# Performance work log

Hardware: AMD Instinct MI355X
Metric: run time of the kernel (lower is better)

The kernel has to match this reference:

```python
import jax, jax.numpy as jnp
import numpy as np

N_NODES = 100000


def _gcn_conv(h, src, dst, norm, W, b):
    # h: [N, F_in] -> [N, F_out]; aggregate normalized messages over edges
    h = h @ W                                   # transform first (cheaper messages)
    msg = h[src] * norm[:, None]                # [E_tot, F_out]
    agg = jax.ops.segment_sum(msg, dst, num_segments=N_NODES)
    return agg + b


def setup_inputs() -> dict:
    key = jax.random.key(0)
    k1, k2, k3, k4 = jax.random.split(key, 4)
    x = jax.random.normal(k1, (N_NODES, 256), dtype=jnp.float32)
    edge_index = jax.random.randint(k2, (2, 1600000), 0, N_NODES, dtype=jnp.int64)
    W1 = jax.random.normal(k3, (256, 128), dtype=jnp.float32) * (1.0 / np.sqrt(256))
    b1 = jnp.zeros((128,), dtype=jnp.float32)
    W2 = jax.random.normal(k4, (128, 40), dtype=jnp.float32) * (1.0 / np.sqrt(128))
    b2 = jnp.zeros((40,), dtype=jnp.float32)
    return {"x": x, "edge_index": edge_index, "W1": W1, "b1": b1, "W2": W2, "b2": b2}


def reference(x, edge_index, W1, b1, W2, b2):
    # add self-loops
    loop = jnp.arange(N_NODES, dtype=edge_index.dtype)
    src = jnp.concatenate([edge_index[0], loop])
    dst = jnp.concatenate([edge_index[1], loop])
    # symmetric normalization D^{-1/2} (A+I) D^{-1/2}
    deg = jax.ops.segment_sum(jnp.ones_like(dst, dtype=x.dtype), dst, num_segments=N_NODES)
    dinv = jax.lax.rsqrt(jnp.maximum(deg, 1.0))
    norm = dinv[src] * dinv[dst]                # [E_tot]

    h = _gcn_conv(x, src, dst, norm, W1, b1)
    h = jax.nn.relu(h)                          # dropout p=0 / eval -> identity
    h = _gcn_conv(h, src, dst, norm, W2, b2)
    return jax.nn.log_softmax(h, axis=1)
```

## Files before the change

kernel.cpp:

```cpp
#include <hip/hip_runtime.h>
#include <hip/hip_fp8.h>
#include <math.h>

#define N_NODES 100000
#define N_EDGES 1600000
#define F_IN 256
#define F_H 128
#define F_OUT 40

#define BIN_SHIFT 9
#define BIN_NODES 512
#define NBIN 196
#define CAP 12288
#define CNT_PAD 16
#define PART_CHUNK 8192
#define DEGB 64

typedef __attribute__((ext_vector_type(8))) short bf16x8;
typedef __attribute__((ext_vector_type(4))) float floatx4;
typedef __attribute__((ext_vector_type(2))) float floatx2;
typedef __attribute__((ext_vector_type(2))) unsigned int uintx2;
typedef __attribute__((ext_vector_type(4))) unsigned int uintx4;

__device__ __forceinline__ unsigned short f2bf(float f) {
    unsigned int u = __float_as_uint(f);
    u += 0x7fffu + ((u >> 16) & 1u);
    return (unsigned short)(u >> 16);
}

#if defined(__has_builtin)
#if __has_builtin(__builtin_amdgcn_cvt_pk_fp8_f32)
#define HAVE_PK_ENC 1
#endif
#if __has_builtin(__builtin_amdgcn_cvt_pk_f32_fp8)
#define HAVE_PK_DEC 1
#endif
#if __has_builtin(__builtin_amdgcn_cvt_f32_fp8)
#define HAVE_SC_DEC 1
#endif
#endif

__device__ __forceinline__ unsigned char f2f8(float f) {
#ifdef HAVE_PK_ENC
    int r = __builtin_amdgcn_cvt_pk_fp8_f32(f, f, 0, false);
    return (unsigned char)(r & 0xff);
#else
    __hip_fp8_e4m3 t(f);
    return (unsigned char)t.__x;
#endif
}
__device__ __forceinline__ float f82f(unsigned char b) {
#ifdef HAVE_SC_DEC
    return __builtin_amdgcn_cvt_f32_fp8((int)b, 0);
#else
    __hip_fp8_e4m3 t; t.__x = (__hip_fp8_storage_t)b;
    return (float)t;
#endif
}
__device__ __forceinline__ floatx2 f8x2tof(unsigned short u) {
#ifdef HAVE_PK_DEC
    return __builtin_amdgcn_cvt_pk_f32_fp8((int)u, false);
#else
    floatx2 r;
    r.x = f82f((unsigned char)(u & 0xff));
    r.y = f82f((unsigned char)(u >> 8));
    return r;
#endif
}

__device__ __forceinline__ void acc16(uintx4 u, float* a) {
#pragma unroll
    for (int d = 0; d < 4; ++d) {
        floatx2 lo = f8x2tof((unsigned short)(u[d] & 0xffffu));
        floatx2 hi = f8x2tof((unsigned short)(u[d] >> 16));
        a[d * 4 + 0] += lo.x; a[d * 4 + 1] += lo.y;
        a[d * 4 + 2] += hi.x; a[d * 4 + 3] += hi.y;
    }
}

__global__ __launch_bounds__(256) void k_part(const int* __restrict__ eidx,
                                              int* __restrict__ gcnt,
                                              unsigned int* __restrict__ parts) {
    __shared__ int hist[4][NBIN];
    __shared__ int sbase[NBIN];
    __shared__ int rcnt[NBIN];
    const int tid = threadIdx.x;
    const int wv = tid >> 6;
    for (int i = tid; i < NBIN; i += 256) {
        hist[0][i] = 0; hist[1][i] = 0; hist[2][i] = 0; hist[3][i] = 0; rcnt[i] = 0;
    }
    __syncthreads();
    const int e0 = blockIdx.x * PART_CHUNK;
    const int e1 = min(e0 + PART_CHUNK, N_EDGES);
    for (int e = e0 + tid; e < e1; e += 256) {
        int d = eidx[N_EDGES + e];
        atomicAdd(&hist[wv][d >> BIN_SHIFT], 1);
    }
    __syncthreads();
    for (int b = tid; b < NBIN; b += 256) {
        int tot = hist[0][b] + hist[1][b] + hist[2][b] + hist[3][b];
        int old = atomicAdd(&gcnt[b * CNT_PAD], tot);
        sbase[b] = b * CAP + old;
    }
    __syncthreads();
    for (int e = e0 + tid; e < e1; e += 256) {
        int d = eidx[N_EDGES + e];
        int s = eidx[e];
        int b = d >> BIN_SHIFT;
        int r = atomicAdd(&rcnt[b], 1);
        parts[sbase[b] + r] = ((unsigned int)s << BIN_SHIFT) | (unsigned int)(d & (BIN_NODES - 1));
    }
}

__global__ __launch_bounds__(256) void k_build(const unsigned int* __restrict__ parts,
                                               const int* __restrict__ gcnt,
                                               int* __restrict__ rowptr,
                                               float* __restrict__ dinv,
                                               int* __restrict__ csr_src) {
    __shared__ int deg[4][BIN_NODES];
    __shared__ int cur[BIN_NODES];
    __shared__ int scan[256];
    const int tid = threadIdx.x;
    const int wv = tid >> 6;
    const int g = blockIdx.x;

    scan[tid] = (tid < NBIN) ? gcnt[tid * CNT_PAD] : 0;
    __syncthreads();
    for (int off = 1; off < 256; off <<= 1) {
        int v = 0;
        if (tid >= off) v = scan[tid - off];
        __syncthreads();
        if (tid >= off) scan[tid] += v;
        __syncthreads();
    }
    const int binBase = (g == 0) ? 0 : scan[g - 1];
    const int cntg = scan[g] - binBase;

    for (int i = tid; i < BIN_NODES; i += 256) {
        deg[0][i] = 0; deg[1][i] = 0; deg[2][i] = 0; deg[3][i] = 0;
    }
    __syncthreads();

    const unsigned int* pp = parts + (size_t)g * CAP;
    for (int i = tid; i < cntg; i += 256)
        atomicAdd(&deg[wv][pp[i] & (BIN_NODES - 1)], 1);
    __syncthreads();

    const int n0 = 2 * tid, n1 = 2 * tid + 1;
    const int d0 = deg[0][n0] + deg[1][n0] + deg[2][n0] + deg[3][n0];
    const int d1 = deg[0][n1] + deg[1][n1] + deg[2][n1] + deg[3][n1];
    scan[tid] = d0 + d1;
    __syncthreads();
    for (int off = 1; off < 256; off <<= 1) {
        int v = 0;
        if (tid >= off) v = scan[tid - off];
        __syncthreads();
        if (tid >= off) scan[tid] += v;
        __syncthreads();
    }
    const int pre = (tid == 0) ? 0 : scan[tid - 1];
    const int p0 = binBase + pre;
    const int p1 = p0 + d0;
    const int node0 = g * BIN_NODES + n0;
    if (node0 < N_NODES)     { rowptr[node0]     = p0; dinv[node0]     = rsqrtf((float)d0 + 1.0f); }
    if (node0 + 1 < N_NODES) { rowptr[node0 + 1] = p1; dinv[node0 + 1] = rsqrtf((float)d1 + 1.0f); }
    cur[n0] = p0;
    cur[n1] = p1;
    __syncthreads();

    for (int i = tid; i < cntg; i += 256) {
        unsigned int u = pp[i];
        int pos = atomicAdd(&cur[u & (BIN_NODES - 1)], 1);
        csr_src[pos] = (int)(u >> BIN_SHIFT);
    }
    if (g == NBIN - 1 && tid == 0) rowptr[N_NODES] = N_EDGES;
}

__global__ __launch_bounds__(256) void k_dhist(const int* __restrict__ rowptr,
                                               int* __restrict__ dcnt) {
    __shared__ int h[4][DEGB];
    const int tid = threadIdx.x;
    const int wv = tid >> 6;
    if (tid < DEGB) { h[0][tid] = 0; h[1][tid] = 0; h[2][tid] = 0; h[3][tid] = 0; }
    __syncthreads();
    const int base = blockIdx.x * 1024;
#pragma unroll
    for (int j = 0; j < 4; ++j) {
        int i = base + j * 256 + tid;
        if (i < N_NODES) {
            int d = min(rowptr[i + 1] - rowptr[i], DEGB - 1);
            atomicAdd(&h[wv][d], 1);
        }
    }
    __syncthreads();
    if (tid < DEGB) {
        int tot = h[0][tid] + h[1][tid] + h[2][tid] + h[3][tid];
        if (tot) atomicAdd(&dcnt[tid * CNT_PAD], tot);
    }
}

__global__ void k_dscan(int* dcnt) {
    if (threadIdx.x == 0) {
        int run = 0;
        for (int i = 0; i < DEGB; ++i) {
            int c = dcnt[i * CNT_PAD];
            dcnt[i * CNT_PAD] = run;
            run += c;
        }
    }
}

__global__ __launch_bounds__(256) void k_dscat(const int* __restrict__ rowptr,
                                               int* __restrict__ dcnt,
                                               int* __restrict__ perm) {
    __shared__ int h[4][DEGB];
    __shared__ int base[DEGB];
    __shared__ int lr[DEGB];
    const int tid = threadIdx.x;
    const int wv = tid >> 6;
    if (tid < DEGB) {
        h[0][tid] = 0; h[1][tid] = 0; h[2][tid] = 0; h[3][tid] = 0; lr[tid] = 0;
    }
    __syncthreads();
    const int nb = blockIdx.x * 1024;
    int dg[4];
#pragma unroll
    for (int j = 0; j < 4; ++j) {
        int i = nb + j * 256 + tid;
        dg[j] = -1;
        if (i < N_NODES) {
            dg[j] = min(rowptr[i + 1] - rowptr[i], DEGB - 1);
            atomicAdd(&h[wv][dg[j]], 1);
        }
    }
    __syncthreads();
    if (tid < DEGB) {
        int tot = h[0][tid] + h[1][tid] + h[2][tid] + h[3][tid];
        base[tid] = tot ? atomicAdd(&dcnt[tid * CNT_PAD], tot) : 0;
    }
    __syncthreads();
#pragma unroll
    for (int j = 0; j < 4; ++j) {
        int i = nb + j * 256 + tid;
        if (dg[j] >= 0) {
            int r = atomicAdd(&lr[dg[j]], 1);
            perm[base[dg[j]] + r] = i;
        }
    }
}

__global__ void k_cvt_w(const float* __restrict__ W1, const float* __restrict__ W2,
                        short* __restrict__ W1t, short* __restrict__ W2t,
                        int* __restrict__ gcnt, int* __restrict__ dcnt) {
    int b = blockIdx.x, t = threadIdx.x;
    if (b < 128) {
        int idx = b * 256 + t;
        int n = idx >> 8, k = idx & 255;
        W1t[n * 256 + k] = (short)f2bf(W1[k * 128 + n]);
    } else {
        int idx = (b - 128) * 256 + t;
        if (idx < 48 * 128) {
            int n = idx >> 7, k = idx & 127;
            float v = (n < F_OUT) ? W2[k * F_OUT + n] : 0.f;
            W2t[n * 128 + k] = (short)f2bf(v);
        }
        if (idx < NBIN * CNT_PAD) gcnt[idx] = 0;
        if (idx < DEGB * CNT_PAD) dcnt[idx] = 0;
    }
}

__global__ __launch_bounds__(256) void k_gemm1_mfma(const float* __restrict__ x,
                                                    const short* __restrict__ W1t,
                                                    const float* __restrict__ dinv,
                                                    unsigned char* __restrict__ h1f8) {
    __shared__ short As[128 * 40];
    __shared__ short Bs[128 * 264];
    __shared__ float Ds[128];
    const int tid = threadIdx.x;
    const int row0 = blockIdx.x * 128;
    const int w = tid >> 6, l = tid & 63;
    const int l15 = l & 15, q = l >> 4;
    const int ar = tid >> 1;
    const int ak = (tid & 1) * 16;

    {
        const int n = tid >> 1;
        const int kh = (tid & 1) * 128;
#pragma unroll
        for (int i = 0; i < 16; ++i)
            *(bf16x8*)&Bs[n * 264 + kh + i * 8] = *(const bf16x8*)&W1t[n * 256 + kh + i * 8];
    }
    if (tid < 128) {
        int r = row0 + tid;
        Ds[tid] = (r < N_NODES) ? dinv[r] : 0.f;
    }

    floatx4 acc[2][8];
#pragma unroll
    for (int a = 0; a < 2; ++a)
#pragma unroll
        for (int nt = 0; nt < 8; ++nt) acc[a][nt] = (floatx4)0.f;

    const bool arow_ok = (row0 + ar) < N_NODES;
    const float* xp = x + (size_t)(row0 + ar) * F_IN;

    for (int k0 = 0; k0 < F_IN; k0 += 32) {
        bf16x8 av0 = (bf16x8)0, av1 = (bf16x8)0;
        if (arow_ok) {
            floatx4 f0 = *(const floatx4*)(xp + k0 + ak);
            floatx4 f1 = *(const floatx4*)(xp + k0 + ak + 4);
            floatx4 f2 = *(const floatx4*)(xp + k0 + ak + 8);
            floatx4 f3 = *(const floatx4*)(xp + k0 + ak + 12);
            av0[0] = (short)f2bf(f0[0]); av0[1] = (short)f2bf(f0[1]);
            av0[2] = (short)f2bf(f0[2]); av0[3] = (short)f2bf(f0[3]);
            av0[4] = (short)f2bf(f1[0]); av0[5] = (short)f2bf(f1[1]);
            av0[6] = (short)f2bf(f1[2]); av0[7] = (short)f2bf(f1[3]);
            av1[0] = (short)f2bf(f2[0]); av1[1] = (short)f2bf(f2[1]);
            av1[2] = (short)f2bf(f2[2]); av1[3] = (short)f2bf(f2[3]);
            av1[4] = (short)f2bf(f3[0]); av1[5] = (short)f2bf(f3[1]);
            av1[6] = (short)f2bf(f3[2]); av1[7] = (short)f2bf(f3[3]);
        }
        __syncthreads();
        *(bf16x8*)&As[ar * 40 + ak]     = av0;
        *(bf16x8*)&As[ar * 40 + ak + 8] = av1;
        __syncthreads();

        bf16x8 af[2], bfr[8];
#pragma unroll
        for (int a = 0; a < 2; ++a)
            af[a] = *(const bf16x8*)&As[((w * 2 + a) * 16 + l15) * 40 + q * 8];
#pragma unroll
        for (int nt = 0; nt < 8; ++nt)
            bfr[nt] = *(const bf16x8*)&Bs[(nt * 16 + l15) * 264 + k0 + q * 8];
#pragma unroll
        for (int a = 0; a < 2; ++a)
#pragma unroll
            for (int nt = 0; nt < 8; ++nt)
                acc[a][nt] = __builtin_amdgcn_mfma_f32_16x16x32_bf16(af[a], bfr[nt], acc[a][nt], 0, 0, 0);
    }
#pragma unroll
    for (int a = 0; a < 2; ++a) {
#pragma unroll
        for (int r = 0; r < 4; ++r) {
            const int rl = (w * 2 + a) * 16 + q * 4 + r;
            const int row = row0 + rl;
            if (row < N_NODES) {
                const float ds = Ds[rl];
                unsigned char* hp = h1f8 + (size_t)row * F_H;
#pragma unroll
                for (int nt = 0; nt < 8; ++nt)
                    hp[nt * 16 + l15] = f2f8(acc[a][nt][r] * ds);
            }
        }
    }
}

__global__ __launch_bounds__(256) void k_spmm1(const int* __restrict__ rowptr,
                                               const int* __restrict__ csr_src,
                                               const int* __restrict__ perm,
                                               const uintx4* __restrict__ h1d4,
                                               const float* __restrict__ dinv,
                                               const float* __restrict__ b1,
                                               unsigned short* __restrict__ agg1b) {
    const int slot = threadIdx.x >> 3;
    const int p = threadIdx.x & 7;
    const int gid = blockIdx.x * 32 + slot;
    const int node = perm[gid];

    const int beg = rowptr[node];
    const int end = rowptr[node + 1];
    const float dv = dinv[node];

    float accA[16], accB[16];
#pragma unroll
    for (int jj = 0; jj < 16; ++jj) { accA[jj] = 0.f; accB[jj] = 0.f; }
    acc16(h1d4[(size_t)node * 8 + p], accA);

    int i = beg;
    for (; i + 3 < end; i += 4) {
        int s0 = csr_src[i], s1 = csr_src[i + 1], s2 = csr_src[i + 2], s3 = csr_src[i + 3];
        uintx4 u0 = h1d4[(size_t)s0 * 8 + p];
        uintx4 u1 = h1d4[(size_t)s1 * 8 + p];
        uintx4 u2 = h1d4[(size_t)s2 * 8 + p];
        uintx4 u3 = h1d4[(size_t)s3 * 8 + p];
        acc16(u0, accA); acc16(u1, accB);
        acc16(u2, accA); acc16(u3, accB);
    }
    for (; i < end; ++i)
        acc16(h1d4[(size_t)csr_src[i] * 8 + p], accA);

    const float* bp = b1 + 16 * p;
    unsigned int ow[8];
#pragma unroll
    for (int jj = 0; jj < 8; ++jj) {
        float v0 = fmaf(accA[2 * jj]     + accB[2 * jj],     dv, bp[2 * jj]);
        float v1 = fmaf(accA[2 * jj + 1] + accB[2 * jj + 1], dv, bp[2 * jj + 1]);
        v0 = v0 > 0.f ? v0 : 0.f;
        v1 = v1 > 0.f ? v1 : 0.f;
        ow[jj] = ((unsigned int)f2bf(v1) << 16) | f2bf(v0);
    }
    uintx4* op = (uintx4*)(agg1b + (size_t)node * F_H) + 2 * p;
    uintx4 o0, o1;
    o0[0] = ow[0]; o0[1] = ow[1]; o0[2] = ow[2]; o0[3] = ow[3];
    o1[0] = ow[4]; o1[1] = ow[5]; o1[2] = ow[6]; o1[3] = ow[7];
    op[0] = o0;
    op[1] = o1;
}

__global__ __launch_bounds__(256) void k_gemm2_mfma(const unsigned short* __restrict__ agg1b,
                                                    const short* __restrict__ W2t,
                                                    const float* __restrict__ dinv,
                                                    unsigned char* __restrict__ h2f8) {
    __shared__ short As[128 * 40];
    __shared__ short Bs[48 * 136];
    __shared__ float Ds[128];
    const int tid = threadIdx.x;
    const int bidr = blockIdx.x;
    const int kx = bidr & 7, jx = bidr >> 3;
    const int cb = (kx < 6) ? (kx * 98 + jx) : (6 * 98 + (kx - 6) * 97 + jx);
    const int row0 = cb * 128;
    const int w = tid >> 6, l = tid & 63;
    const int l15 = l & 15, q = l >> 4;
    const int ar = tid >> 1;
    const int ak = (tid & 1) * 16;

#pragma unroll
    for (int i = 0; i < 3; ++i) {
        int c = tid * 3 + i;
        int n = c >> 4, koff = (c & 15) * 8;
        *(bf16x8*)&Bs[n * 136 + koff] = *(const bf16x8*)&W2t[n * 128 + koff];
    }
    if (tid < 128) {
        int r = row0 + tid;
        Ds[tid] = (r < N_NODES) ? dinv[r] : 0.f;
    }

    floatx4 acc[2][3];
#pragma unroll
    for (int a = 0; a < 2; ++a)
#pragma unroll
        for (int nt = 0; nt < 3; ++nt) acc[a][nt] = (floatx4)0.f;

    const bool arow_ok = (row0 + ar) < N_NODES;
    const unsigned short* ap = agg1b + (size_t)(row0 + ar) * F_H;

    for (int k0 = 0; k0 < F_H; k0 += 32) {
        bf16x8 a0, a1;
        if (arow_ok) {
            a0 = *(const bf16x8*)(ap + k0 + ak);
            a1 = *(const bf16x8*)(ap + k0 + ak + 8);
        } else {
            a0 = (bf16x8)0; a1 = (bf16x8)0;
        }
        *(bf16x8*)&As[ar * 40 + ak]     = a0;
        *(bf16x8*)&As[ar * 40 + ak + 8] = a1;
        __syncthreads();

        bf16x8 af[2], bfr[3];
#pragma unroll
        for (int a = 0; a < 2; ++a)
            af[a] = *(const bf16x8*)&As[((w * 2 + a) * 16 + l15) * 40 + q * 8];
#pragma unroll
        for (int nt = 0; nt < 3; ++nt)
            bfr[nt] = *(const bf16x8*)&Bs[(nt * 16 + l15) * 136 + k0 + q * 8];
#pragma unroll
        for (int a = 0; a < 2; ++a)
#pragma unroll
            for (int nt = 0; nt < 3; ++nt)
                acc[a][nt] = __builtin_amdgcn_mfma_f32_16x16x32_bf16(af[a], bfr[nt], acc[a][nt], 0, 0, 0);
        __syncthreads();
    }
#pragma unroll
    for (int a = 0; a < 2; ++a) {
#pragma unroll
        for (int nt = 0; nt < 3; ++nt) {
            int col = nt * 16 + l15;
#pragma unroll
            for (int r = 0; r < 4; ++r) {
                int rl = (w * 2 + a) * 16 + q * 4 + r;
                int row = row0 + rl;
                if (row < N_NODES && col < F_OUT)
                    h2f8[(size_t)row * F_OUT + col] = f2f8(acc[a][nt][r] * Ds[rl]);
            }
        }
    }
}

__global__ __launch_bounds__(256) void k_spmm2_lsm(const int* __restrict__ rowptr,
                                                   const int* __restrict__ csr_src,
                                                   const int* __restrict__ perm,
                                                   const unsigned int* __restrict__ h2d,
                                                   const float* __restrict__ dinv,
                                                   const float* __restrict__ b2,
                                                   float* __restrict__ out) {
    const int qid = threadIdx.x >> 4;
    const int p = threadIdx.x & 15;
    const int gid = blockIdx.x * 16 + qid;
    const int node = perm[gid];
    bool valid = (p < 10);
    int beg = 0, end = 0;
    if (valid) { beg = rowptr[node]; end = rowptr[node + 1]; }
    float dv = dinv[node];

    float A0 = 0.f, A1 = 0.f, A2 = 0.f, A3 = 0.f;
    float B0 = 0.f, B1 = 0.f, B2 = 0.f, B3 = 0.f;
    if (valid) {
        unsigned int su = h2d[(size_t)node * 10 + p];
        floatx2 t0 = f8x2tof((unsigned short)(su & 0xffffu));
        floatx2 t1 = f8x2tof((unsigned short)(su >> 16));
        A0 = t0.x; A1 = t0.y; A2 = t1.x; A3 = t1.y;
    }
    int i = beg;
    for (; i + 1 < end; i += 2) {
        int s0 = csr_src[i], s1 = csr_src[i + 1];
        unsigned int u0 = h2d[(size_t)s0 * 10 + p];
        unsigned int u1 = h2d[(size_t)s1 * 10 + p];
        floatx2 a01 = f8x2tof((unsigned short)(u0 & 0xffffu));
        floatx2 a23 = f8x2tof((unsigned short)(u0 >> 16));
        floatx2 b01 = f8x2tof((unsigned short)(u1 & 0xffffu));
        floatx2 b23 = f8x2tof((unsigned short)(u1 >> 16));
        A0 += a01.x; A1 += a01.y; A2 += a23.x; A3 += a23.y;
        B0 += b01.x; B1 += b01.y; B2 += b23.x; B3 += b23.y;
    }
    if (i < end) {
        unsigned int u0 = h2d[(size_t)csr_src[i] * 10 + p];
        floatx2 a01 = f8x2tof((unsigned short)(u0 & 0xffffu));
        floatx2 a23 = f8x2tof((unsigned short)(u0 >> 16));
        A0 += a01.x; A1 += a01.y; A2 += a23.x; A3 += a23.y;
    }

    float v0 = -INFINITY, v1 = -INFINITY, v2 = -INFINITY, v3 = -INFINITY;
    if (valid) {
        float4 bb = *(const float4*)&b2[4 * p];
        v0 = fmaf(A0 + B0, dv, bb.x);
        v1 = fmaf(A1 + B1, dv, bb.y);
        v2 = fmaf(A2 + B2, dv, bb.z);
        v3 = fmaf(A3 + B3, dv, bb.w);
    }
    float m = fmaxf(fmaxf(v0, v1), fmaxf(v2, v3));
#pragma unroll
    for (int off = 1; off < 16; off <<= 1) m = fmaxf(m, __shfl_xor(m, off, 16));
    float e = 0.f;
    if (valid) e = expf(v0 - m) + expf(v1 - m) + expf(v2 - m) + expf(v3 - m);
#pragma unroll
    for (int off = 1; off < 16; off <<= 1) e += __shfl_xor(e, off, 16);
    if (valid) {
        float ls = logf(e);
        floatx4 o;
        o[0] = v0 - m - ls; o[1] = v1 - m - ls; o[2] = v2 - m - ls; o[3] = v3 - m - ls;
        __builtin_nontemporal_store(o, (floatx4*)&out[(size_t)node * F_OUT + 4 * p]);
    }
}

extern "C" void kernel_launch(void* const* d_in, const int* in_sizes, int n_in,
                              void* d_out, int out_size, void* d_ws, size_t ws_size,
                              hipStream_t stream) {
    const float* x = (const float*)d_in[0];
    const int* eidx = (const int*)d_in[1];
    const float* W1 = (const float*)d_in[2];
    const float* b1 = (const float*)d_in[3];
    const float* W2 = (const float*)d_in[4];
    const float* b2 = (const float*)d_in[5];
    float* out = (float*)d_out;

    char* ws = (char*)d_ws;
    int*   gcnt      = (int*)  (ws);
    int*   dcnt      = (int*)  (ws + 16384);
    int*   rowptr    = (int*)  (ws + 400512);
    int*   perm      = (int*)  (ws + 800528);
    int*   csr_src   = (int*)  (ws + 1200528);
    float* dinv      = (float*)(ws + 7600528);
    short* W1t       = (short*)(ws + 8000528);
    short* W2t       = (short*)(ws + 8066064);
    unsigned char*  h1f8  = (unsigned char*) (ws + 8078352);
    unsigned short* agg1b = (unsigned short*)(ws + 20878352);
    unsigned int*   parts = (unsigned int*)  (ws + 20878352);
    unsigned char*  h2f8  = (unsigned char*) (ws + 46478352);

    k_cvt_w<<<152, 256, 0, stream>>>(W1, W2, W1t, W2t, gcnt, dcnt);
    k_part<<<(N_EDGES + PART_CHUNK - 1) / PART_CHUNK, 256, 0, stream>>>(eidx, gcnt, parts);
    k_build<<<NBIN, 256, 0, stream>>>(parts, gcnt, rowptr, dinv, csr_src);

    k_dhist<<<(N_NODES + 1023) / 1024, 256, 0, stream>>>(rowptr, dcnt);
    k_dscan<<<1, 64, 0, stream>>>(dcnt);
    k_dscat<<<(N_NODES + 1023) / 1024, 256, 0, stream>>>(rowptr, dcnt, perm);

    k_gemm1_mfma<<<(N_NODES + 127) / 128, 256, 0, stream>>>(x, W1t, dinv, h1f8);
    k_spmm1<<<3125, 256, 0, stream>>>(rowptr, csr_src, perm,
                                      (const uintx4*)h1f8, dinv, b1, agg1b);
    k_gemm2_mfma<<<782, 256, 0, stream>>>(agg1b, W2t, dinv, h2f8);
    k_spmm2_lsm<<<6250, 256, 0, stream>>>(rowptr, csr_src, perm,
                                          (const unsigned int*)h2f8, dinv, b2, out);
}
```

Before: 351.1 us.

## Split layer-1 gather into four feature planes for cache locality

GEMM1 now writes the fp8 hidden features as four planar 32-column slices, and the layer-1 SpMM runs four times, once per slice. Each pass gathers a 3.2 MB table that fits in cache better than the full 12.8 MB table. The cost is re-reading the CSR row pointers and indices four times and adding three kernel launches. Layer-2 SpMM also drops the degree-sorted permutation and walks nodes in natural order.

```diff
diff --git a/kernel.cpp b/kernel.cpp
--- a/kernel.cpp
+++ b/kernel.cpp
@@ -272,7 +272,7 @@
 __global__ __launch_bounds__(256) void k_gemm1_mfma(const float* __restrict__ x,
                                                     const short* __restrict__ W1t,
                                                     const float* __restrict__ dinv,
-                                                    unsigned char* __restrict__ h1f8) {
+                                                    unsigned char* __restrict__ h1q) {
     __shared__ short As[128 * 40];
     __shared__ short Bs[128 * 264];
     __shared__ float Ds[128];
@@ -346,25 +346,26 @@
             const int row = row0 + rl;
             if (row < N_NODES) {
                 const float ds = Ds[rl];
-                unsigned char* hp = h1f8 + (size_t)row * F_H;
 #pragma unroll
                 for (int nt = 0; nt < 8; ++nt)
-                    hp[nt * 16 + l15] = f2f8(acc[a][nt][r] * ds);
+                    h1q[((size_t)(nt >> 1) * N_NODES + row) * 32 + (nt & 1) * 16 + l15]
+                        = f2f8(acc[a][nt][r] * ds);
             }
         }
     }
 }
 
-__global__ __launch_bounds__(256) void k_spmm1(const int* __restrict__ rowptr,
-                                               const int* __restrict__ csr_src,
-                                               const int* __restrict__ perm,
-                                               const uintx4* __restrict__ h1d4,
-                                               const float* __restrict__ dinv,
-                                               const float* __restrict__ b1,
-                                               unsigned short* __restrict__ agg1b) {
-    const int slot = threadIdx.x >> 3;
-    const int p = threadIdx.x & 7;
-    const int gid = blockIdx.x * 32 + slot;
+__global__ __launch_bounds__(256) void k_spmm1_q(const int* __restrict__ rowptr,
+                                                 const int* __restrict__ csr_src,
+                                                 const int* __restrict__ perm,
+                                                 const uintx4* __restrict__ hq,
+                                                 const float* __restrict__ dinv,
+                                                 const float* __restrict__ b1p,
+                                                 unsigned short* __restrict__ aggp) {
+    const int slot = threadIdx.x >> 1;
+    const int pq = threadIdx.x & 1;
+    const int gid = blockIdx.x * 128 + slot;
+    if (gid >= N_NODES) return;
     const int node = perm[gid];
 
     const int beg = rowptr[node];
@@ -374,22 +375,22 @@
     float accA[16], accB[16];
 #pragma unroll
     for (int jj = 0; jj < 16; ++jj) { accA[jj] = 0.f; accB[jj] = 0.f; }
-    acc16(h1d4[(size_t)node * 8 + p], accA);
+    acc16(hq[(size_t)node * 2 + pq], accA);
 
     int i = beg;
     for (; i + 3 < end; i += 4) {
         int s0 = csr_src[i], s1 = csr_src[i + 1], s2 = csr_src[i + 2], s3 = csr_src[i + 3];
-        uintx4 u0 = h1d4[(size_t)s0 * 8 + p];
-        uintx4 u1 = h1d4[(size_t)s1 * 8 + p];
-        uintx4 u2 = h1d4[(size_t)s2 * 8 + p];
-        uintx4 u3 = h1d4[(size_t)s3 * 8 + p];
+        uintx4 u0 = hq[(size_t)s0 * 2 + pq];
+        uintx4 u1 = hq[(size_t)s1 * 2 + pq];
+        uintx4 u2 = hq[(size_t)s2 * 2 + pq];
+        uintx4 u3 = hq[(size_t)s3 * 2 + pq];
         acc16(u0, accA); acc16(u1, accB);
         acc16(u2, accA); acc16(u3, accB);
     }
     for (; i < end; ++i)
-        acc16(h1d4[(size_t)csr_src[i] * 8 + p], accA);
-
-    const float* bp = b1 + 16 * p;
+        acc16(hq[(size_t)csr_src[i] * 2 + pq], accA);
+
+    const float* bp = b1p + 16 * pq;
     unsigned int ow[8];
 #pragma unroll
     for (int jj = 0; jj < 8; ++jj) {
@@ -399,7 +400,7 @@
         v1 = v1 > 0.f ? v1 : 0.f;
         ow[jj] = ((unsigned int)f2bf(v1) << 16) | f2bf(v0);
     }
-    uintx4* op = (uintx4*)(agg1b + (size_t)node * F_H) + 2 * p;
+    uintx4* op = (uintx4*)(aggp + (size_t)node * F_H + pq * 16);
     uintx4 o0, o1;
     o0[0] = ow[0]; o0[1] = ow[1]; o0[2] = ow[2]; o0[3] = ow[3];
     o1[0] = ow[4]; o1[1] = ow[5]; o1[2] = ow[6]; o1[3] = ow[7];
@@ -488,24 +489,24 @@
 
 __global__ __launch_bounds__(256) void k_spmm2_lsm(const int* __restrict__ rowptr,
                                                    const int* __restrict__ csr_src,
-                                                   const int* __restrict__ perm,
                                                    const unsigned int* __restrict__ h2d,
                                                    const float* __restrict__ dinv,
                                                    const float* __restrict__ b2,
                                                    float* __restrict__ out) {
     const int qid = threadIdx.x >> 4;
     const int p = threadIdx.x & 15;
-    const int gid = blockIdx.x * 16 + qid;
-    const int node = perm[gid];
-    bool valid = (p < 10);
+    int node = blockIdx.x * 16 + qid;
+    bool nvalid = node < N_NODES;
+    bool valid = nvalid && (p < 10);
+    int nd = nvalid ? node : 0;
     int beg = 0, end = 0;
-    if (valid) { beg = rowptr[node]; end = rowptr[node + 1]; }
-    float dv = dinv[node];
+    if (valid) { beg = rowptr[nd]; end = rowptr[nd + 1]; }
+    float dv = dinv[nd];
 
     float A0 = 0.f, A1 = 0.f, A2 = 0.f, A3 = 0.f;
     float B0 = 0.f, B1 = 0.f, B2 = 0.f, B3 = 0.f;
     if (valid) {
-        unsigned int su = h2d[(size_t)node * 10 + p];
+        unsigned int su = h2d[(size_t)nd * 10 + p];
         floatx2 t0 = f8x2tof((unsigned short)(su & 0xffffu));
         floatx2 t1 = f8x2tof((unsigned short)(su >> 16));
         A0 = t0.x; A1 = t0.y; A2 = t1.x; A3 = t1.y;
@@ -572,7 +573,7 @@
     float* dinv      = (float*)(ws + 7600528);
     short* W1t       = (short*)(ws + 8000528);
     short* W2t       = (short*)(ws + 8066064);
-    unsigned char*  h1f8  = (unsigned char*) (ws + 8078352);
+    unsigned char*  h1q   = (unsigned char*) (ws + 8078352);
     unsigned short* agg1b = (unsigned short*)(ws + 20878352);
     unsigned int*   parts = (unsigned int*)  (ws + 20878352);
     unsigned char*  h2f8  = (unsigned char*) (ws + 46478352);
@@ -585,10 +586,15 @@
     k_dscan<<<1, 64, 0, stream>>>(dcnt);
     k_dscat<<<(N_NODES + 1023) / 1024, 256, 0, stream>>>(rowptr, dcnt, perm);
 
-    k_gemm1_mfma<<<(N_NODES + 127) / 128, 256, 0, stream>>>(x, W1t, dinv, h1f8);
-    k_spmm1<<<3125, 256, 0, stream>>>(rowptr, csr_src, perm,
-                                      (const uintx4*)h1f8, dinv, b1, agg1b);
+    k_gemm1_mfma<<<(N_NODES + 127) / 128, 256, 0, stream>>>(x, W1t, dinv, h1q);
+
+    for (int pl = 0; pl < 4; ++pl)
+        k_spmm1_q<<<(N_NODES + 127) / 128, 256, 0, stream>>>(
+            rowptr, csr_src, perm,
+            (const uintx4*)(h1q + (size_t)pl * N_NODES * 32),
+            dinv, b1 + pl * 32, agg1b + pl * 32);
+
     k_gemm2_mfma<<<782, 256, 0, stream>>>(agg1b, W2t, dinv, h2f8);
-    k_spmm2_lsm<<<6250, 256, 0, stream>>>(rowptr, csr_src, perm,
-                                          (const unsigned int*)h2f8, dinv, b2, out);
-}
+    k_spmm2_lsm<<<(N_NODES + 15) / 16, 256, 0, stream>>>(rowptr, csr_src,
+                                                         (const unsigned int*)h2f8, dinv, b2, out);
+}
```

After: 405.7 us. 15.6% more time.
